# Kernel tuning notes

Measured on AMD Instinct MI355X. Metric: run time of the kernel, lower is better.

## Reference

```python
import jax, jax.numpy as jnp
import numpy as np

EPS = 1e-5


def setup_inputs() -> dict:
    key = jax.random.key(0)
    ks = jax.random.split(key, 5)
    N, E, D, L = 10000, 160000, 512, 3
    x = jax.random.normal(ks[0], (N, D), dtype=jnp.float32)
    src = jax.random.randint(ks[1], (E,), 0, N, dtype=jnp.int64)
    dst = jax.random.randint(ks[2], (E,), 0, N, dtype=jnp.int64)
    gamma = jnp.ones((L, D), dtype=jnp.float32)
    beta = jnp.zeros((L, D), dtype=jnp.float32)
    # glorot-ish scale so ReLU stack stays well-conditioned
    W = jax.random.normal(ks[3], (L, D, D), dtype=jnp.float32) * (1.0 / np.sqrt(D))
    b = jnp.zeros((L, D), dtype=jnp.float32)
    return {"x": x, "src": src, "dst": dst, "gamma": gamma, "beta": beta, "W": W, "b": b}


def reference(x, src, dst, gamma, beta, W, b):
    N = x.shape[0]
    ones = jnp.ones(src.shape[0], dtype=x.dtype)
    # DGL GraphConv norm='both': src side uses out-degree, dst side uses in-degree
    out_deg = jnp.clip(jax.ops.segment_sum(ones, src, num_segments=N), 1.0)
    in_deg = jnp.clip(jax.ops.segment_sum(ones, dst, num_segments=N), 1.0)
    src_norm = (out_deg ** -0.5)[:, None]  # [N,1]
    dst_norm = (in_deg ** -0.5)[:, None]   # [N,1]
    n_layers = gamma.shape[0]
    for i in range(n_layers):
        # BatchNorm1d (training mode: batch mean, biased variance)
        mu = jnp.mean(x, axis=0)
        var = jnp.var(x, axis=0)
        x = (x - mu) * jax.lax.rsqrt(var + EPS) * gamma[i] + beta[i]
        h = x * src_norm
        agg = jax.ops.segment_sum(h[src], dst, num_segments=N) * dst_norm
        x = jax.nn.relu(agg @ W[i] + b[i])
    return x
```

## Files before the change

### kernel.cpp

```cpp
#include <hip/hip_runtime.h>
#include <hip/hip_bf16.h>

constexpr int N = 10000;
constexpr int D = 512;
constexpr int E = 160000;
constexpr int L = 3;
constexpr float EPS = 1e-5f;

typedef _Float16 half8 __attribute__((ext_vector_type(8)));
typedef _Float16 half2v __attribute__((ext_vector_type(2)));
typedef float floatx4 __attribute__((ext_vector_type(4)));

__device__ __forceinline__ void glds16(const _Float16* g, _Float16* l) {
    __builtin_amdgcn_global_load_lds(
        (const __attribute__((address_space(1))) uint32_t*)(g),
        (__attribute__((address_space(3))) uint32_t*)(l),
        16, 0, 0);
}

constexpr int DEG_BLOCKS  = (E + 255) / 256;
constexpr int STAT_BLOCKS = 500;
constexpr int TW_BLOCKS   = L * 256;
constexpr int MEGA_BLOCKS = DEG_BLOCKS + STAT_BLOCKS + TW_BLOCKS;

__global__ __launch_bounds__(256) void mega_setup(
    const int* __restrict__ src, const int* __restrict__ dst,
    const float* __restrict__ x, const float* __restrict__ W,
    int* __restrict__ out_deg, int* __restrict__ in_deg,
    float* __restrict__ stats0, _Float16* __restrict__ Wt) {
    __shared__ float tb[32][33];
    int bid = blockIdx.x;
    int tid = threadIdx.x;
    if (bid < DEG_BLOCKS) {
        int e = bid * 256 + tid;
        if (e < E) {
            atomicAdd(&out_deg[src[e]], 1);
            atomicAdd(&in_deg[dst[e]], 1);
        }
    } else if (bid < DEG_BLOCKS + STAT_BLOCKS) {
        int b = bid - DEG_BLOCKS;
        int r0 = b * 20;
        int r1 = r0 + 20; if (r1 > N) r1 = N;
        int c2 = tid * 2;
        float s0 = 0.f, s1 = 0.f, q0 = 0.f, q1 = 0.f;
        for (int r = r0; r < r1; ++r) {
            float2 v = *(const float2*)(x + (size_t)r * D + c2);
            s0 += v.x; q0 += v.x * v.x;
            s1 += v.y; q1 += v.y * v.y;
        }
        atomicAdd(&stats0[c2], s0);
        atomicAdd(&stats0[c2 + 1], s1);
        atomicAdd(&stats0[D + c2], q0);
        atomicAdd(&stats0[D + c2 + 1], q1);
    } else {
        int b = bid - DEG_BLOCKS - STAT_BLOCKS;
        int l = b >> 8;
        int t = b & 255;
        int k0 = (t >> 4) * 32, n0 = (t & 15) * 32;
        int tx = tid & 31, ty = tid >> 5;
        const float* Wl = W + (size_t)l * D * D;
        _Float16* Wtl = Wt + (size_t)l * D * D;
        for (int i = 0; i < 32; i += 8)
            tb[ty + i][tx] = Wl[(size_t)(k0 + ty + i) * D + n0 + tx];
        __syncthreads();
        for (int i = 0; i < 32; i += 8)
            Wtl[(size_t)(n0 + ty + i) * D + k0 + tx] = (_Float16)tb[tx][ty + i];
    }
}

__global__ void scan_indeg(const int* __restrict__ in_deg,
                           const int* __restrict__ out_deg,
                           int* __restrict__ off, int* __restrict__ cursor,
                           float* __restrict__ src_norm, float* __restrict__ dst_norm) {
    __shared__ int lsum[1024];
    int t = threadIdx.x;
    const int chunk = (N + 1023) / 1024;
    int start = t * chunk;
    int end = start + chunk; if (end > N) end = N;
    int s = 0;
    for (int i = start; i < end; ++i) s += in_deg[i];
    lsum[t] = s;
    __syncthreads();
    for (int d = 1; d < 1024; d <<= 1) {
        int v = (t >= d) ? lsum[t - d] : 0;
        __syncthreads();
        lsum[t] += v;
        __syncthreads();
    }
    int excl = (t == 0) ? 0 : lsum[t - 1];
    for (int i = start; i < end; ++i) {
        off[i] = excl;
        cursor[i] = excl;
        excl += in_deg[i];
        int od = out_deg[i]; if (od < 1) od = 1;
        int id = in_deg[i];  if (id < 1) id = 1;
        src_norm[i] = rsqrtf((float)od);
        dst_norm[i] = rsqrtf((float)id);
    }
    if (t == 1023) off[N] = lsum[1023];
}

constexpr int CONV_BLOCKS = 500;
__global__ __launch_bounds__(256) void csr_fill_conv(
    const int* __restrict__ src, const int* __restrict__ dst,
    const float* __restrict__ x, const float* __restrict__ src_norm,
    int* __restrict__ cursor, int* __restrict__ csr_src,
    float* __restrict__ T, _Float16* __restrict__ x16) {
    int bid = blockIdx.x;
    int tid = threadIdx.x;
    if (bid < DEG_BLOCKS) {
        int e = bid * 256 + tid;
        if (e < E) {
            int s = src[e], d = dst[e];
            int pos = atomicAdd(&cursor[d], 1);
            csr_src[pos] = s;
            atomicAdd(&T[d], src_norm[s]);
        }
    } else {
        int b = bid - DEG_BLOCKS;
        int r0 = b * 20;
        int r1 = r0 + 20; if (r1 > N) r1 = N;
        int c2 = tid * 2;
        for (int r = r0; r < r1; ++r) {
            float sn = src_norm[r];
            float2 v = *(const float2*)(x + (size_t)r * D + c2);
            half2v h;
            h[0] = (_Float16)(v.x * sn);
            h[1] = (_Float16)(v.y * sn);
            *(half2v*)(x16 + (size_t)r * D + c2) = h;
        }
    }
}

__global__ __launch_bounds__(256) void aggregate_pre(
    const _Float16* __restrict__ xs, const int* __restrict__ off,
    const int* __restrict__ csr_src, const float* __restrict__ T,
    const float* __restrict__ dst_norm, const float* __restrict__ stats,
    const float* __restrict__ gamma, const float* __restrict__ beta,
    _Float16* __restrict__ agg) {
    int wid = blockIdx.x * 4 + (threadIdx.x >> 6);
    int lane = threadIdx.x & 63;
    int c0 = lane * 8;
    const _Float16* xp = xs + c0;

    int e0 = __builtin_amdgcn_readfirstlane(off[wid]);
    int e1 = __builtin_amdgcn_readfirstlane(off[wid + 1]);

    float a[8] = {}, b2[8] = {};
    int e = e0;
    for (; e + 6 <= e1; e += 6) {
        int s0 = csr_src[e];
        int s1 = csr_src[e + 1];
        int s2 = csr_src[e + 2];
        int s3 = csr_src[e + 3];
        int s4 = csr_src[e + 4];
        int s5 = csr_src[e + 5];
        half8 v0 = *(const half8*)(xp + (size_t)s0 * D);
        half8 v1 = *(const half8*)(xp + (size_t)s1 * D);
        half8 v2 = *(const half8*)(xp + (size_t)s2 * D);
        half8 v3 = *(const half8*)(xp + (size_t)s3 * D);
        half8 v4 = *(const half8*)(xp + (size_t)s4 * D);
        half8 v5 = *(const half8*)(xp + (size_t)s5 * D);
#pragma unroll
        for (int k = 0; k < 8; ++k) {
            a[k]  += (float)v0[k] + (float)v2[k] + (float)v4[k];
            b2[k] += (float)v1[k] + (float)v3[k] + (float)v5[k];
        }
    }
    for (; e < e1; ++e) {
        int s0 = csr_src[e];
        half8 v0 = *(const half8*)(xp + (size_t)s0 * D);
#pragma unroll
        for (int k = 0; k < 8; ++k) a[k] += (float)v0[k];
    }

    float t = T[wid];
    float dn = dst_norm[wid];
    const float invN = 1.0f / (float)N;
    half8 o;
#pragma unroll
    for (int k = 0; k < 8; ++k) {
        int c = c0 + k;
        float mu = stats[c] * invN;
        float var = stats[D + c] * invN - mu * mu;
        float sc = gamma[c] * rsqrtf(var + EPS);
        float sh = beta[c] - mu * sc;
        o[k] = (_Float16)(dn * (sc * (a[k] + b2[k]) + sh * t));
    }
    *(half8*)(agg + (size_t)wid * D + c0) = o;
}

template <typename OutT, bool STATS>
__global__ __launch_bounds__(256) void mm_f16_relu(
    const _Float16* __restrict__ A, const _Float16* __restrict__ Bt,
    const float* __restrict__ bias, OutT* __restrict__ C, int M,
    float* __restrict__ stats, const float* __restrict__ src_norm) {
    __shared__ __align__(16) _Float16 As[128 * 32];
    __shared__ __align__(16) _Float16 Bs[128 * 32];
    const int tid  = threadIdx.x;
    const int wave = tid >> 6;
    const int lane = tid & 63;
    const int quad = lane >> 4;
    const int l16  = lane & 15;
    const int row0 = blockIdx.x * 128;
    const int col0 = blockIdx.y * 128;
    const int wm = (wave & 1) * 64;
    const int wn = (wave >> 1) * 64;
    const int sr = lane >> 2;
    const int sc = (lane & 3) * 8;

    int ar0 = row0 + wave * 32 + sr;
    int ar1 = ar0 + 16;
    if (ar0 >= M) ar0 = M - 1;
    if (ar1 >= M) ar1 = M - 1;
    const _Float16* gA0 = A + (size_t)ar0 * D + sc;
    const _Float16* gA1 = A + (size_t)ar1 * D + sc;
    const _Float16* gB0 = Bt + (size_t)(col0 + wave * 32 + sr) * D + sc;
    const _Float16* gB1 = Bt + (size_t)(col0 + wave * 32 + 16 + sr) * D + sc;
    _Float16* lA0 = As + (wave * 32) * 32;
    _Float16* lA1 = As + (wave * 32 + 16) * 32;
    _Float16* lB0 = Bs + (wave * 32) * 32;
    _Float16* lB1 = Bs + (wave * 32 + 16) * 32;

    floatx4 acc[4][4] = {};

    for (int k0 = 0; k0 < D; k0 += 32) {
        __syncthreads();
        glds16(gA0 + k0, lA0);
        glds16(gA1 + k0, lA1);
        glds16(gB0 + k0, lB0);
        glds16(gB1 + k0, lB1);
        __syncthreads();
        half8 af[4], bf[4];
        for (int i = 0; i < 4; ++i)
            af[i] = *(const half8*)(As + (wm + i * 16 + l16) * 32 + quad * 8);
        for (int j = 0; j < 4; ++j)
            bf[j] = *(const half8*)(Bs + (wn + j * 16 + l16) * 32 + quad * 8);
        for (int i = 0; i < 4; ++i)
            for (int j = 0; j < 4; ++j)
                acc[i][j] = __builtin_amdgcn_mfma_f32_16x16x32_f16(
                    af[i], bf[j], acc[i][j], 0, 0, 0);
    }

    float s[4] = {}, q[4] = {};
    for (int i = 0; i < 4; ++i) {
        for (int r = 0; r < 4; ++r) {
            int row = row0 + wm + i * 16 + quad * 4 + r;
            bool valid = row < M;
            float sn = 1.0f;
            if (STATS && valid) sn = src_norm[row];
            for (int j = 0; j < 4; ++j) {
                int col = col0 + wn + j * 16 + l16;
                float v = acc[i][j][r] + bias[col];
                v = v > 0.f ? v : 0.f;
                if (valid) {
                    if (STATS) {
                        C[(size_t)row * D + col] = (OutT)(v * sn);
                        s[j] += v; q[j] += v * v;
                    } else {
                        C[(size_t)row * D + col] = (OutT)v;
                    }
                }
            }
        }
    }
    if (STATS) {
        for (int j = 0; j < 4; ++j) {
            float sv = s[j], qv = q[j];
            sv += __shfl_xor(sv, 16); sv += __shfl_xor(sv, 32);
            qv += __shfl_xor(qv, 16); qv += __shfl_xor(qv, 32);
            if (quad == 0) {
                int col = col0 + wn + j * 16 + l16;
                atomicAdd(&stats[col], sv);
                atomicAdd(&stats[D + col], qv);
            }
        }
    }
}

extern "C" void kernel_launch(void* const* d_in, const int* in_sizes, int n_in,
                              void* d_out, int out_size, void* d_ws, size_t ws_size,
                              hipStream_t stream) {
    const float* x_in  = (const float*)d_in[0];
    const int*   src   = (const int*)d_in[1];
    const int*   dst   = (const int*)d_in[2];
    const float* gamma = (const float*)d_in[3];
    const float* beta  = (const float*)d_in[4];
    const float* W     = (const float*)d_in[5];
    const float* b     = (const float*)d_in[6];
    float* out = (float*)d_out;

    char* p = (char*)d_ws;
    _Float16* x16 = (_Float16*)p;  p += (size_t)N * D * 2;
    _Float16* agg = (_Float16*)p;  p += (size_t)N * D * 2;
    _Float16* Wt  = (_Float16*)p;  p += (size_t)L * D * D * 2;
    float* src_norm = (float*)p;   p += (size_t)N * 4;
    float* dst_norm = (float*)p;   p += (size_t)N * 4;
    int* out_deg   = (int*)p;      p += (size_t)N * 4;
    int* in_deg    = (int*)p;      p += (size_t)N * 4;
    float* stats0  = (float*)p;    p += 2 * D * 4;
    float* stats1  = (float*)p;    p += 2 * D * 4;
    float* stats2  = (float*)p;    p += 2 * D * 4;
    float* T       = (float*)p;    p += (size_t)N * 4;
    int* csr_off   = (int*)p;      p += (size_t)(N + 1) * 4;
    int* cursor    = (int*)p;      p += (size_t)N * 4;
    int* csr_src   = (int*)p;      p += (size_t)E * 4;

    float* stats_in[3] = {stats0, stats1, stats2};

    hipMemsetAsync(out_deg, 0, (3 * (size_t)N + 6 * D) * sizeof(int), stream);
    mega_setup<<<MEGA_BLOCKS, 256, 0, stream>>>(src, dst, x_in, W,
                                                out_deg, in_deg, stats0, Wt);
    scan_indeg<<<1, 1024, 0, stream>>>(in_deg, out_deg, csr_off, cursor,
                                       src_norm, dst_norm);
    csr_fill_conv<<<DEG_BLOCKS + CONV_BLOCKS, 256, 0, stream>>>(
        src, dst, x_in, src_norm, cursor, csr_src, T, x16);

    dim3 mm_grid((N + 127) / 128, D / 128);
    const int agg_blocks = (N + 3) / 4;

    for (int l = 0; l < L; ++l) {
        const float* gl  = gamma + (size_t)l * D;
        const float* bl  = beta + (size_t)l * D;
        const _Float16* Wl = Wt + (size_t)l * D * D;
        const float* bil = b + (size_t)l * D;

        aggregate_pre<<<agg_blocks, 256, 0, stream>>>(
            x16, csr_off, csr_src, T, dst_norm, stats_in[l], gl, bl, agg);
        if (l == L - 1) {
            mm_f16_relu<float, false><<<mm_grid, 256, 0, stream>>>(
                agg, Wl, bil, out, N, nullptr, nullptr);
        } else {
            mm_f16_relu<_Float16, true><<<mm_grid, 256, 0, stream>>>(
                agg, Wl, bil, x16, N, stats_in[l + 1], src_norm);
        }
    }
}
```

Measured before the change: 302.9 us.

## Fuse whole GCN pipeline into one persistent cooperative kernel with grid syncs

```diff
diff --git a/kernel.cpp b/kernel.cpp
--- a/kernel.cpp
+++ b/kernel.cpp
@@ -1,11 +1,20 @@
 #include <hip/hip_runtime.h>
 #include <hip/hip_bf16.h>
+#include <hip/hip_cooperative_groups.h>
+
+namespace cg = cooperative_groups;
 
 constexpr int N = 10000;
 constexpr int D = 512;
 constexpr int E = 160000;
 constexpr int L = 3;
 constexpr float EPS = 1e-5f;
+
+constexpr int DEG_T  = (E + 255) / 256;
+constexpr int CONV_T = 250;
+constexpr int TW_T   = L * 256;
+constexpr int MM_TX  = (N + 127) / 128;
+constexpr int MM_T   = MM_TX * (D / 128);
 
 typedef _Float16 half8 __attribute__((ext_vector_type(8)));
 typedef _Float16 half2v __attribute__((ext_vector_type(2)));
@@ -18,321 +27,326 @@
         16, 0, 0);
 }
 
-constexpr int DEG_BLOCKS  = (E + 255) / 256;
-constexpr int STAT_BLOCKS = 500;
-constexpr int TW_BLOCKS   = L * 256;
-constexpr int MEGA_BLOCKS = DEG_BLOCKS + STAT_BLOCKS + TW_BLOCKS;
-
-__global__ __launch_bounds__(256) void mega_setup(
-    const int* __restrict__ src, const int* __restrict__ dst,
-    const float* __restrict__ x, const float* __restrict__ W,
-    int* __restrict__ out_deg, int* __restrict__ in_deg,
-    float* __restrict__ stats0, _Float16* __restrict__ Wt) {
-    __shared__ float tb[32][33];
-    int bid = blockIdx.x;
-    int tid = threadIdx.x;
-    if (bid < DEG_BLOCKS) {
-        int e = bid * 256 + tid;
+struct KParams {
+    const int* src; const int* dst;
+    const float* x; const float* W;
+    const float* gamma; const float* beta; const float* b;
+    float* out;
+    _Float16* x16; _Float16* agg; _Float16* Wt;
+    float* src_norm; float* dst_norm; float* csr_norm;
+    int* out_deg; int* in_deg;
+    float* stats0; float* stats1; float* stats2;
+    int* csr_off; int* cursor; int* csr_src;
+};
+
+__global__ __launch_bounds__(1024) void gcn_fused(KParams P) {
+    cg::grid_group grid = cg::this_grid();
+    const int bid  = blockIdx.x;
+    const int tid  = threadIdx.x;
+    const int st   = tid >> 8;
+    const int vt   = tid & 255;
+    const int wv   = tid >> 6;
+    const int wv4  = wv & 3;
+    const int lane = tid & 63;
+    const int gw   = (wv << 8) | bid;
+
+    __shared__ __align__(16) _Float16 mmA[4][128 * 32];
+    __shared__ __align__(16) _Float16 mmB[4][128 * 32];
+    __shared__ int lsum[1024];
+
+    {
+        int n = 2 * N + 6 * D;
+        int i = bid * 1024 + tid;
+        if (i < n) P.out_deg[i] = 0;
+    }
+    grid.sync();
+
+    for (int task = st * 256 + bid; task < DEG_T + CONV_T + TW_T; task += 1024) {
+        if (task < DEG_T) {
+            int e = task * 256 + vt;
+            if (e < E) {
+                atomicAdd(&P.out_deg[P.src[e]], 1);
+                atomicAdd(&P.in_deg[P.dst[e]], 1);
+            }
+        } else if (task < DEG_T + CONV_T) {
+            int ct = task - DEG_T;
+            int r0 = ct * 40;
+            int r1 = r0 + 40; if (r1 > N) r1 = N;
+            int c2 = vt * 2;
+            float s0 = 0.f, s1 = 0.f, q0 = 0.f, q1 = 0.f;
+            for (int r = r0; r < r1; ++r) {
+                float2 v = *(const float2*)(P.x + (size_t)r * D + c2);
+                s0 += v.x; q0 += v.x * v.x;
+                s1 += v.y; q1 += v.y * v.y;
+                half2v h; h[0] = (_Float16)v.x; h[1] = (_Float16)v.y;
+                *(half2v*)(P.x16 + (size_t)r * D + c2) = h;
+            }
+            atomicAdd(&P.stats0[c2], s0);
+            atomicAdd(&P.stats0[c2 + 1], s1);
+            atomicAdd(&P.stats0[D + c2], q0);
+            atomicAdd(&P.stats0[D + c2 + 1], q1);
+        } else {
+            int tt = task - DEG_T - CONV_T;
+            int l = tt >> 8;
+            int t = tt & 255;
+            int k0 = (t >> 4) * 32, n0 = (t & 15) * 32;
+            int tx = vt & 31, ty = vt >> 5;
+            const float* Wl = P.W + (size_t)l * D * D;
+            _Float16* Wtl = P.Wt + (size_t)l * D * D;
+#pragma unroll
+            for (int i2 = 0; i2 < 32; i2 += 8)
+                Wtl[(size_t)(n0 + ty + i2) * D + k0 + tx] =
+                    (_Float16)Wl[(size_t)(k0 + tx) * D + n0 + ty + i2];
+        }
+    }
+    grid.sync();
+
+    if (bid == 0) {
+        int t = tid;
+        const int chunk = (N + 1023) / 1024;
+        int start = t * chunk;
+        int end = start + chunk; if (end > N) end = N;
+        int s = 0;
+        for (int i = start; i < end; ++i) s += P.in_deg[i];
+        lsum[t] = s;
+        __syncthreads();
+        for (int d = 1; d < 1024; d <<= 1) {
+            int v = (t >= d) ? lsum[t - d] : 0;
+            __syncthreads();
+            lsum[t] += v;
+            __syncthreads();
+        }
+        int excl = (t == 0) ? 0 : lsum[t - 1];
+        for (int i = start; i < end; ++i) {
+            P.csr_off[i] = excl;
+            P.cursor[i] = excl;
+            excl += P.in_deg[i];
+            int od = P.out_deg[i]; if (od < 1) od = 1;
+            int id = P.in_deg[i];  if (id < 1) id = 1;
+            P.src_norm[i] = rsqrtf((float)od);
+            P.dst_norm[i] = rsqrtf((float)id);
+        }
+        if (t == 1023) P.csr_off[N] = lsum[1023];
+    }
+    grid.sync();
+
+    for (int task = st * 256 + bid; task < DEG_T; task += 1024) {
+        int e = task * 256 + vt;
         if (e < E) {
-            atomicAdd(&out_deg[src[e]], 1);
-            atomicAdd(&in_deg[dst[e]], 1);
-        }
-    } else if (bid < DEG_BLOCKS + STAT_BLOCKS) {
-        int b = bid - DEG_BLOCKS;
-        int r0 = b * 20;
-        int r1 = r0 + 20; if (r1 > N) r1 = N;
-        int c2 = tid * 2;
-        float s0 = 0.f, s1 = 0.f, q0 = 0.f, q1 = 0.f;
-        for (int r = r0; r < r1; ++r) {
-            float2 v = *(const float2*)(x + (size_t)r * D + c2);
-            s0 += v.x; q0 += v.x * v.x;
-            s1 += v.y; q1 += v.y * v.y;
-        }
-        atomicAdd(&stats0[c2], s0);
-        atomicAdd(&stats0[c2 + 1], s1);
-        atomicAdd(&stats0[D + c2], q0);
-        atomicAdd(&stats0[D + c2 + 1], q1);
-    } else {
-        int b = bid - DEG_BLOCKS - STAT_BLOCKS;
-        int l = b >> 8;
-        int t = b & 255;
-        int k0 = (t >> 4) * 32, n0 = (t & 15) * 32;
-        int tx = tid & 31, ty = tid >> 5;
-        const float* Wl = W + (size_t)l * D * D;
-        _Float16* Wtl = Wt + (size_t)l * D * D;
-        for (int i = 0; i < 32; i += 8)
-            tb[ty + i][tx] = Wl[(size_t)(k0 + ty + i) * D + n0 + tx];
-        __syncthreads();
-        for (int i = 0; i < 32; i += 8)
-            Wtl[(size_t)(n0 + ty + i) * D + k0 + tx] = (_Float16)tb[tx][ty + i];
-    }
-}
-
-__global__ void scan_indeg(const int* __restrict__ in_deg,
-                           const int* __restrict__ out_deg,
-                           int* __restrict__ off, int* __restrict__ cursor,
-                           float* __restrict__ src_norm, float* __restrict__ dst_norm) {
-    __shared__ int lsum[1024];
-    int t = threadIdx.x;
-    const int chunk = (N + 1023) / 1024;
-    int start = t * chunk;
-    int end = start + chunk; if (end > N) end = N;
-    int s = 0;
-    for (int i = start; i < end; ++i) s += in_deg[i];
-    lsum[t] = s;
-    __syncthreads();
-    for (int d = 1; d < 1024; d <<= 1) {
-        int v = (t >= d) ? lsum[t - d] : 0;
-        __syncthreads();
-        lsum[t] += v;
-        __syncthreads();
-    }
-    int excl = (t == 0) ? 0 : lsum[t - 1];
-    for (int i = start; i < end; ++i) {
-        off[i] = excl;
-        cursor[i] = excl;
-        excl += in_deg[i];
-        int od = out_deg[i]; if (od < 1) od = 1;
-        int id = in_deg[i];  if (id < 1) id = 1;
-        src_norm[i] = rsqrtf((float)od);
-        dst_norm[i] = rsqrtf((float)id);
-    }
-    if (t == 1023) off[N] = lsum[1023];
-}
-
-constexpr int CONV_BLOCKS = 500;
-__global__ __launch_bounds__(256) void csr_fill_conv(
-    const int* __restrict__ src, const int* __restrict__ dst,
-    const float* __restrict__ x, const float* __restrict__ src_norm,
-    int* __restrict__ cursor, int* __restrict__ csr_src,
-    float* __restrict__ T, _Float16* __restrict__ x16) {
-    int bid = blockIdx.x;
-    int tid = threadIdx.x;
-    if (bid < DEG_BLOCKS) {
-        int e = bid * 256 + tid;
-        if (e < E) {
-            int s = src[e], d = dst[e];
-            int pos = atomicAdd(&cursor[d], 1);
-            csr_src[pos] = s;
-            atomicAdd(&T[d], src_norm[s]);
-        }
-    } else {
-        int b = bid - DEG_BLOCKS;
-        int r0 = b * 20;
-        int r1 = r0 + 20; if (r1 > N) r1 = N;
-        int c2 = tid * 2;
-        for (int r = r0; r < r1; ++r) {
-            float sn = src_norm[r];
-            float2 v = *(const float2*)(x + (size_t)r * D + c2);
-            half2v h;
-            h[0] = (_Float16)(v.x * sn);
-            h[1] = (_Float16)(v.y * sn);
-            *(half2v*)(x16 + (size_t)r * D + c2) = h;
-        }
-    }
-}
-
-__global__ __launch_bounds__(256) void aggregate_pre(
-    const _Float16* __restrict__ xs, const int* __restrict__ off,
-    const int* __restrict__ csr_src, const float* __restrict__ T,
-    const float* __restrict__ dst_norm, const float* __restrict__ stats,
-    const float* __restrict__ gamma, const float* __restrict__ beta,
-    _Float16* __restrict__ agg) {
-    int wid = blockIdx.x * 4 + (threadIdx.x >> 6);
-    int lane = threadIdx.x & 63;
-    int c0 = lane * 8;
-    const _Float16* xp = xs + c0;
-
-    int e0 = __builtin_amdgcn_readfirstlane(off[wid]);
-    int e1 = __builtin_amdgcn_readfirstlane(off[wid + 1]);
-
-    float a[8] = {}, b2[8] = {};
-    int e = e0;
-    for (; e + 6 <= e1; e += 6) {
-        int s0 = csr_src[e];
-        int s1 = csr_src[e + 1];
-        int s2 = csr_src[e + 2];
-        int s3 = csr_src[e + 3];
-        int s4 = csr_src[e + 4];
-        int s5 = csr_src[e + 5];
-        half8 v0 = *(const half8*)(xp + (size_t)s0 * D);
-        half8 v1 = *(const half8*)(xp + (size_t)s1 * D);
-        half8 v2 = *(const half8*)(xp + (size_t)s2 * D);
-        half8 v3 = *(const half8*)(xp + (size_t)s3 * D);
-        half8 v4 = *(const half8*)(xp + (size_t)s4 * D);
-        half8 v5 = *(const half8*)(xp + (size_t)s5 * D);
-#pragma unroll
-        for (int k = 0; k < 8; ++k) {
-            a[k]  += (float)v0[k] + (float)v2[k] + (float)v4[k];
-            b2[k] += (float)v1[k] + (float)v3[k] + (float)v5[k];
-        }
-    }
-    for (; e < e1; ++e) {
-        int s0 = csr_src[e];
-        half8 v0 = *(const half8*)(xp + (size_t)s0 * D);
-#pragma unroll
-        for (int k = 0; k < 8; ++k) a[k] += (float)v0[k];
-    }
-
-    float t = T[wid];
-    float dn = dst_norm[wid];
-    const float invN = 1.0f / (float)N;
-    half8 o;
-#pragma unroll
-    for (int k = 0; k < 8; ++k) {
-        int c = c0 + k;
-        float mu = stats[c] * invN;
-        float var = stats[D + c] * invN - mu * mu;
-        float sc = gamma[c] * rsqrtf(var + EPS);
-        float sh = beta[c] - mu * sc;
-        o[k] = (_Float16)(dn * (sc * (a[k] + b2[k]) + sh * t));
-    }
-    *(half8*)(agg + (size_t)wid * D + c0) = o;
-}
-
-template <typename OutT, bool STATS>
-__global__ __launch_bounds__(256) void mm_f16_relu(
-    const _Float16* __restrict__ A, const _Float16* __restrict__ Bt,
-    const float* __restrict__ bias, OutT* __restrict__ C, int M,
-    float* __restrict__ stats, const float* __restrict__ src_norm) {
-    __shared__ __align__(16) _Float16 As[128 * 32];
-    __shared__ __align__(16) _Float16 Bs[128 * 32];
-    const int tid  = threadIdx.x;
-    const int wave = tid >> 6;
-    const int lane = tid & 63;
-    const int quad = lane >> 4;
-    const int l16  = lane & 15;
-    const int row0 = blockIdx.x * 128;
-    const int col0 = blockIdx.y * 128;
-    const int wm = (wave & 1) * 64;
-    const int wn = (wave >> 1) * 64;
-    const int sr = lane >> 2;
-    const int sc = (lane & 3) * 8;
-
-    int ar0 = row0 + wave * 32 + sr;
-    int ar1 = ar0 + 16;
-    if (ar0 >= M) ar0 = M - 1;
-    if (ar1 >= M) ar1 = M - 1;
-    const _Float16* gA0 = A + (size_t)ar0 * D + sc;
-    const _Float16* gA1 = A + (size_t)ar1 * D + sc;
-    const _Float16* gB0 = Bt + (size_t)(col0 + wave * 32 + sr) * D + sc;
-    const _Float16* gB1 = Bt + (size_t)(col0 + wave * 32 + 16 + sr) * D + sc;
-    _Float16* lA0 = As + (wave * 32) * 32;
-    _Float16* lA1 = As + (wave * 32 + 16) * 32;
-    _Float16* lB0 = Bs + (wave * 32) * 32;
-    _Float16* lB1 = Bs + (wave * 32 + 16) * 32;
-
-    floatx4 acc[4][4] = {};
-
-    for (int k0 = 0; k0 < D; k0 += 32) {
-        __syncthreads();
-        glds16(gA0 + k0, lA0);
-        glds16(gA1 + k0, lA1);
-        glds16(gB0 + k0, lB0);
-        glds16(gB1 + k0, lB1);
-        __syncthreads();
-        half8 af[4], bf[4];
-        for (int i = 0; i < 4; ++i)
-            af[i] = *(const half8*)(As + (wm + i * 16 + l16) * 32 + quad * 8);
-        for (int j = 0; j < 4; ++j)
-            bf[j] = *(const half8*)(Bs + (wn + j * 16 + l16) * 32 + quad * 8);
-        for (int i = 0; i < 4; ++i)
-            for (int j = 0; j < 4; ++j)
-                acc[i][j] = __builtin_amdgcn_mfma_f32_16x16x32_f16(
-                    af[i], bf[j], acc[i][j], 0, 0, 0);
-    }
-
-    float s[4] = {}, q[4] = {};
-    for (int i = 0; i < 4; ++i) {
-        for (int r = 0; r < 4; ++r) {
-            int row = row0 + wm + i * 16 + quad * 4 + r;
-            bool valid = row < M;
-            float sn = 1.0f;
-            if (STATS && valid) sn = src_norm[row];
-            for (int j = 0; j < 4; ++j) {
-                int col = col0 + wn + j * 16 + l16;
-                float v = acc[i][j][r] + bias[col];
-                v = v > 0.f ? v : 0.f;
-                if (valid) {
-                    if (STATS) {
-                        C[(size_t)row * D + col] = (OutT)(v * sn);
-                        s[j] += v; q[j] += v * v;
-                    } else {
-                        C[(size_t)row * D + col] = (OutT)v;
+            int s = P.src[e];
+            int d = P.dst[e];
+            int pos = atomicAdd(&P.cursor[d], 1);
+            P.csr_src[pos] = s;
+            P.csr_norm[pos] = P.src_norm[s];
+        }
+    }
+    grid.sync();
+
+    for (int l = 0; l < L; ++l) {
+        const float* stats = (l == 0) ? P.stats0 : (l == 1) ? P.stats1 : P.stats2;
+        const float* gl = P.gamma + (size_t)l * D;
+        const float* bl = P.beta + (size_t)l * D;
+
+        {
+            int c0 = lane * 8;
+            const _Float16* xp = P.x16 + c0;
+            for (int wid = gw; wid < N; wid += 4096) {
+                int e0 = __builtin_amdgcn_readfirstlane(P.csr_off[wid]);
+                int e1 = __builtin_amdgcn_readfirstlane(P.csr_off[wid + 1]);
+                float a[8] = {};
+                float tsum = 0.f;
+                int e = e0;
+                for (; e + 8 <= e1; e += 8) {
+                    int s0 = P.csr_src[e + 0];
+                    int s1 = P.csr_src[e + 1];
+                    int s2 = P.csr_src[e + 2];
+                    int s3 = P.csr_src[e + 3];
+                    int s4 = P.csr_src[e + 4];
+                    int s5 = P.csr_src[e + 5];
+                    int s6 = P.csr_src[e + 6];
+                    int s7 = P.csr_src[e + 7];
+                    float n0 = P.csr_norm[e + 0];
+                    float n1 = P.csr_norm[e + 1];
+                    float n2 = P.csr_norm[e + 2];
+                    float n3 = P.csr_norm[e + 3];
+                    float n4 = P.csr_norm[e + 4];
+                    float n5 = P.csr_norm[e + 5];
+                    float n6 = P.csr_norm[e + 6];
+                    float n7 = P.csr_norm[e + 7];
+                    half8 v0 = *(const half8*)(xp + (size_t)s0 * D);
+                    half8 v1 = *(const half8*)(xp + (size_t)s1 * D);
+                    half8 v2 = *(const half8*)(xp + (size_t)s2 * D);
+                    half8 v3 = *(const half8*)(xp + (size_t)s3 * D);
+                    half8 v4 = *(const half8*)(xp + (size_t)s4 * D);
+                    half8 v5 = *(const half8*)(xp + (size_t)s5 * D);
+                    half8 v6 = *(const half8*)(xp + (size_t)s6 * D);
+                    half8 v7 = *(const half8*)(xp + (size_t)s7 * D);
+                    tsum += ((n0 + n1) + (n2 + n3)) + ((n4 + n5) + (n6 + n7));
+#pragma unroll
+                    for (int k = 0; k < 8; ++k) {
+                        float p0 = (float)v0[k] * n0 + (float)v1[k] * n1;
+                        float p1 = (float)v2[k] * n2 + (float)v3[k] * n3;
+                        float p2 = (float)v4[k] * n4 + (float)v5[k] * n5;
+                        float p3 = (float)v6[k] * n6 + (float)v7[k] * n7;
+                        a[k] += (p0 + p1) + (p2 + p3);
                     }
                 }
-            }
-        }
-    }
-    if (STATS) {
-        for (int j = 0; j < 4; ++j) {
-            float sv = s[j], qv = q[j];
-            sv += __shfl_xor(sv, 16); sv += __shfl_xor(sv, 32);
-            qv += __shfl_xor(qv, 16); qv += __shfl_xor(qv, 32);
-            if (quad == 0) {
-                int col = col0 + wn + j * 16 + l16;
-                atomicAdd(&stats[col], sv);
-                atomicAdd(&stats[D + col], qv);
-            }
-        }
+                for (; e < e1; ++e) {
+                    int s0 = P.csr_src[e];
+                    float n0 = P.csr_norm[e];
+                    half8 v0 = *(const half8*)(xp + (size_t)s0 * D);
+                    tsum += n0;
+#pragma unroll
+                    for (int k = 0; k < 8; ++k) a[k] += (float)v0[k] * n0;
+                }
+                float dn = P.dst_norm[wid];
+                const float invN = 1.0f / (float)N;
+                half8 o;
+#pragma unroll
+                for (int k = 0; k < 8; ++k) {
+                    int c = c0 + k;
+                    float mu = stats[c] * invN;
+                    float var = stats[D + c] * invN - mu * mu;
+                    float sc = gl[c] * rsqrtf(var + EPS);
+                    float sh = bl[c] - mu * sc;
+                    o[k] = (_Float16)(dn * (sc * a[k] + sh * tsum));
+                }
+                *(half8*)(P.agg + (size_t)wid * D + c0) = o;
+            }
+        }
+        grid.sync();
+
+        {
+            const int quad = lane >> 4;
+            const int l16  = lane & 15;
+            int gt = st * 256 + bid;
+            bool active = gt < MM_T;
+            int g = active ? gt : 0;
+            int gy = g / MM_TX, gx = g - gy * MM_TX;
+            int row0 = gx * 128, col0 = gy * 128;
+            const int wm = (wv4 & 1) * 64;
+            const int wn = (wv4 >> 1) * 64;
+            const int sr = lane >> 2;
+            const int sc = (lane & 3) * 8;
+            const _Float16* Bt = P.Wt + (size_t)l * D * D;
+            const float* bias = P.b + (size_t)l * D;
+
+            int ar0 = row0 + wv4 * 32 + sr;
+            int ar1 = ar0 + 16;
+            if (ar0 >= N) ar0 = N - 1;
+            if (ar1 >= N) ar1 = N - 1;
+            const _Float16* gA0 = P.agg + (size_t)ar0 * D + sc;
+            const _Float16* gA1 = P.agg + (size_t)ar1 * D + sc;
+            const _Float16* gB0 = Bt + (size_t)(col0 + wv4 * 32 + sr) * D + sc;
+            const _Float16* gB1 = Bt + (size_t)(col0 + wv4 * 32 + 16 + sr) * D + sc;
+            _Float16* lA0 = mmA[st] + (wv4 * 32) * 32;
+            _Float16* lA1 = mmA[st] + (wv4 * 32 + 16) * 32;
+            _Float16* lB0 = mmB[st] + (wv4 * 32) * 32;
+            _Float16* lB1 = mmB[st] + (wv4 * 32 + 16) * 32;
+
+            floatx4 acc[4][4] = {};
+
+            for (int k0 = 0; k0 < D; k0 += 32) {
+                __syncthreads();
+                if (active) {
+                    glds16(gA0 + k0, lA0);
+                    glds16(gA1 + k0, lA1);
+                    glds16(gB0 + k0, lB0);
+                    glds16(gB1 + k0, lB1);
+                }
+                __syncthreads();
+                if (active) {
+                    half8 af[4], bf[4];
+#pragma unroll
+                    for (int i = 0; i < 4; ++i)
+                        af[i] = *(const half8*)(mmA[st] + (wm + i * 16 + l16) * 32 + quad * 8);
+#pragma unroll
+                    for (int j = 0; j < 4; ++j)
+                        bf[j] = *(const half8*)(mmB[st] + (wn + j * 16 + l16) * 32 + quad * 8);
+#pragma unroll
+                    for (int i = 0; i < 4; ++i)
+#pragma unroll
+                        for (int j = 0; j < 4; ++j)
+                            acc[i][j] = __builtin_amdgcn_mfma_f32_16x16x32_f16(
+                                af[i], bf[j], acc[i][j], 0, 0, 0);
+                }
+            }
+
+            if (active) {
+                float s[4] = {}, q[4] = {};
+                bool statsOn = (l < L - 1);
+                float* stats_next = (l == 0) ? P.stats1 : P.stats2;
+#pragma unroll
+                for (int i = 0; i < 4; ++i) {
+#pragma unroll
+                    for (int r = 0; r < 4; ++r) {
+                        int row = row0 + wm + i * 16 + quad * 4 + r;
+                        bool valid = row < N;
+#pragma unroll
+                        for (int j = 0; j < 4; ++j) {
+                            int col = col0 + wn + j * 16 + l16;
+                            float v = acc[i][j][r] + bias[col];
+                            v = v > 0.f ? v : 0.f;
+                            if (valid) {
+                                if (statsOn) {
+                                    P.x16[(size_t)row * D + col] = (_Float16)v;
+                                    s[j] += v; q[j] += v * v;
+                                } else {
+                                    P.out[(size_t)row * D + col] = v;
+                                }
+                            }
+                        }
+                    }
+                }
+                if (statsOn) {
+#pragma unroll
+                    for (int j = 0; j < 4; ++j) {
+                        float sv = s[j], qv = q[j];
+                        sv += __shfl_xor(sv, 16); sv += __shfl_xor(sv, 32);
+                        qv += __shfl_xor(qv, 16); qv += __shfl_xor(qv, 32);
+                        if (quad == 0) {
+                            int col = col0 + wn + j * 16 + l16;
+                            atomicAdd(&stats_next[col], sv);
+                            atomicAdd(&stats_next[D + col], qv);
+                        }
+                    }
+                }
+            }
+        }
+        if (l < L - 1) grid.sync();
     }
 }
 
 extern "C" void kernel_launch(void* const* d_in, const int* in_sizes, int n_in,
                               void* d_out, int out_size, void* d_ws, size_t ws_size,
                               hipStream_t stream) {
-    const float* x_in  = (const float*)d_in[0];
-    const int*   src   = (const int*)d_in[1];
-    const int*   dst   = (const int*)d_in[2];
-    const float* gamma = (const float*)d_in[3];
-    const float* beta  = (const float*)d_in[4];
-    const float* W     = (const float*)d_in[5];
-    const float* b     = (const float*)d_in[6];
-    float* out = (float*)d_out;
+    KParams P;
+    P.x     = (const float*)d_in[0];
+    P.src   = (const int*)d_in[1];
+    P.dst   = (const int*)d_in[2];
+    P.gamma = (const float*)d_in[3];
+    P.beta  = (const float*)d_in[4];
+    P.W     = (const float*)d_in[5];
+    P.b     = (const float*)d_in[6];
+    P.out   = (float*)d_out;
 
     char* p = (char*)d_ws;
-    _Float16* x16 = (_Float16*)p;  p += (size_t)N * D * 2;
-    _Float16* agg = (_Float16*)p;  p += (size_t)N * D * 2;
-    _Float16* Wt  = (_Float16*)p;  p += (size_t)L * D * D * 2;
-    float* src_norm = (float*)p;   p += (size_t)N * 4;
-    float* dst_norm = (float*)p;   p += (size_t)N * 4;
-    int* out_deg   = (int*)p;      p += (size_t)N * 4;
-    int* in_deg    = (int*)p;      p += (size_t)N * 4;
-    float* stats0  = (float*)p;    p += 2 * D * 4;
-    float* stats1  = (float*)p;    p += 2 * D * 4;
-    float* stats2  = (float*)p;    p += 2 * D * 4;
-    float* T       = (float*)p;    p += (size_t)N * 4;
-    int* csr_off   = (int*)p;      p += (size_t)(N + 1) * 4;
-    int* cursor    = (int*)p;      p += (size_t)N * 4;
-    int* csr_src   = (int*)p;      p += (size_t)E * 4;
-
-    float* stats_in[3] = {stats0, stats1, stats2};
-
-    hipMemsetAsync(out_deg, 0, (3 * (size_t)N + 6 * D) * sizeof(int), stream);
-    mega_setup<<<MEGA_BLOCKS, 256, 0, stream>>>(src, dst, x_in, W,
-                                                out_deg, in_deg, stats0, Wt);
-    scan_indeg<<<1, 1024, 0, stream>>>(in_deg, out_deg, csr_off, cursor,
-                                       src_norm, dst_norm);
-    csr_fill_conv<<<DEG_BLOCKS + CONV_BLOCKS, 256, 0, stream>>>(
-        src, dst, x_in, src_norm, cursor, csr_src, T, x16);
-
-    dim3 mm_grid((N + 127) / 128, D / 128);
-    const int agg_blocks = (N + 3) / 4;
-
-    for (int l = 0; l < L; ++l) {
-        const float* gl  = gamma + (size_t)l * D;
-        const float* bl  = beta + (size_t)l * D;
-        const _Float16* Wl = Wt + (size_t)l * D * D;
-        const float* bil = b + (size_t)l * D;
-
-        aggregate_pre<<<agg_blocks, 256, 0, stream>>>(
-            x16, csr_off, csr_src, T, dst_norm, stats_in[l], gl, bl, agg);
-        if (l == L - 1) {
-            mm_f16_relu<float, false><<<mm_grid, 256, 0, stream>>>(
-                agg, Wl, bil, out, N, nullptr, nullptr);
-        } else {
-            mm_f16_relu<_Float16, true><<<mm_grid, 256, 0, stream>>>(
-                agg, Wl, bil, x16, N, stats_in[l + 1], src_norm);
-        }
-    }
+    P.x16 = (_Float16*)p;      p += (size_t)N * D * 2;
+    P.agg = (_Float16*)p;      p += (size_t)N * D * 2;
+    P.Wt  = (_Float16*)p;      p += (size_t)L * D * D * 2;
+    P.src_norm = (float*)p;    p += (size_t)N * 4;
+    P.dst_norm = (float*)p;    p += (size_t)N * 4;
+    P.csr_norm = (float*)p;    p += (size_t)E * 4;
+    P.out_deg = (int*)p;       p += (size_t)N * 4;
+    P.in_deg  = (int*)p;       p += (size_t)N * 4;
+    P.stats0  = (float*)p;     p += 2 * D * 4;
+    P.stats1  = (float*)p;     p += 2 * D * 4;
+    P.stats2  = (float*)p;     p += 2 * D * 4;
+    P.csr_off = (int*)p;       p += (size_t)(N + 1) * 4;
+    P.cursor  = (int*)p;       p += (size_t)N * 4;
+    P.csr_src = (int*)p;       p += (size_t)E * 4;
+
+    void* args[] = {&P};
+    hipLaunchCooperativeKernel((const void*)gcn_fused, dim3(256), dim3(1024),
+                               args, 0, stream);
 }
```

Result: slower. 630.8 us (+108.2%).
